# Optimization experiments

Hardware: AMD Instinct MI355X
Metric: run time of the kernel (lower is better)

Reference implementation:

```python
import jax, jax.numpy as jnp
import numpy as np

D = 64
H = 4
FF = 4  # fourier features
EPS = 1e-5


def _ln(x, g, b):
    m = jnp.mean(x, axis=-1, keepdims=True)
    v = jnp.mean((x - m) ** 2, axis=-1, keepdims=True)
    return (x - m) / jnp.sqrt(v + EPS) * g + b


def setup_inputs() -> dict:
    key = jax.random.key(0)
    ks = jax.random.split(key, 30)
    s = 0.05
    inp = {
        'feats': jax.random.normal(ks[0], (1, 1024, D), jnp.float32),
        'coors': jax.random.normal(ks[1], (1, 1024, 3), jnp.float32),
        'qkv_w': jax.random.normal(ks[2], (D, 3 * D), jnp.float32) * s,
        'out_w': jax.random.normal(ks[3], (D, D), jnp.float32) * s,
        'out_b': jnp.zeros((D,), jnp.float32),
        'edge_w1': jax.random.normal(ks[4], (2 * FF + 1, D), jnp.float32) * s,
        'edge_b1': jnp.zeros((D,), jnp.float32),
        'edge_w2': jax.random.normal(ks[5], (D, D), jnp.float32) * s,
        'edge_b2': jnp.zeros((D,), jnp.float32),
        'coord_w1': jax.random.normal(ks[6], (D, D), jnp.float32) * s,
        'coord_b1': jnp.zeros((D,), jnp.float32),
        'coord_w2': jax.random.normal(ks[7], (D, 1), jnp.float32) * s,
        'coord_b2': jnp.zeros((1,), jnp.float32),
        'gate_w1': jax.random.normal(ks[8], (D, D), jnp.float32) * s,
        'gate_b1': jnp.zeros((D,), jnp.float32),
        'gate_w2': jax.random.normal(ks[9], (D, 1), jnp.float32) * s,
        'gate_b2': jnp.zeros((1,), jnp.float32),
        'ln1_g': jnp.ones((D,), jnp.float32),
        'ln1_b': jnp.zeros((D,), jnp.float32),
        'ln2_g': jnp.ones((D,), jnp.float32),
        'ln2_b': jnp.zeros((D,), jnp.float32),
        'ffn_w1': jax.random.normal(ks[10], (D, 4 * D), jnp.float32) * s,
        'ffn_b1': jnp.zeros((4 * D,), jnp.float32),
        'ffn_w2': jax.random.normal(ks[11], (4 * D, D), jnp.float32) * s,
        'ffn_b2': jnp.zeros((D,), jnp.float32),
    }
    return inp


def reference(feats, coors, qkv_w, out_w, out_b, edge_w1, edge_b1, edge_w2, edge_b2,
              coord_w1, coord_b1, coord_w2, coord_b2, gate_w1, gate_b1, gate_w2, gate_b2,
              ln1_g, ln1_b, ln2_g, ln2_b, ffn_w1, ffn_b1, ffn_w2, ffn_b2):
    B, N, Dm = feats.shape
    x = _ln(feats, ln1_g, ln1_b)  # norm1 (pre-norm; also used as residual base, faithful to source)

    # pairwise relative coords and squared distance
    rel = coors[:, :, None, :] - coors[:, None, :, :]        # [B,N,N,3]
    rd = jnp.sum(rel ** 2, axis=-1, keepdims=True)            # [B,N,N,1]
    freqs = 2.0 ** jnp.arange(FF, dtype=coors.dtype)
    fr = rd / freqs                                           # [B,N,N,FF]
    enc = jnp.concatenate([jnp.sin(fr), jnp.cos(fr), rd], -1) # [B,N,N,2*FF+1]

    # edge MLP (edges=None, edge_dim=0)
    e_ij = jax.nn.silu(enc @ edge_w1 + edge_b1) @ edge_w2 + edge_b2  # [B,N,N,D]

    # attention
    qkv = x @ qkv_w
    q, k, v = jnp.split(qkv, 3, axis=-1)
    hd = Dm // H
    q = q.reshape(B, N, H, hd).transpose(0, 2, 1, 3)
    k = k.reshape(B, N, H, hd).transpose(0, 2, 1, 3)
    v = v.reshape(B, N, H, hd).transpose(0, 2, 1, 3)
    scores = jnp.einsum('bhid,bhjd->bhij', q, k) / jnp.sqrt(jnp.asarray(Dm, q.dtype))
    attn = jax.nn.softmax(scores, axis=-1)                    # [B,H,N,N]
    msg = jnp.einsum('bhij,bhjd->bhid', attn, v)
    msg = msg.transpose(0, 2, 1, 3).reshape(B, N, Dm)
    x = x + (msg @ out_w + out_b)
    x = x + (jax.nn.gelu(_ln(x, ln2_g, ln2_b) @ ffn_w1 + ffn_b1, approximate=False) @ ffn_w2 + ffn_b2)

    # coordinate update
    cw = (jax.nn.silu(e_ij @ coord_w1 + coord_b1) @ coord_w2 + coord_b2)[..., 0]  # [B,N,N]
    cw = cw * jnp.mean(attn, axis=1)
    gate = jax.nn.sigmoid(jax.nn.silu(x @ gate_w1 + gate_b1) @ gate_w2 + gate_b2)  # [B,N,1]
    delta = jnp.einsum('bij,bijd->bid', cw, rel) * gate
    return x, coors + delta
```

## Files before the change

kernel.cpp:

```cpp
#include <hip/hip_runtime.h>
#include <hip/hip_bf16.h>

#define N 1024
#define D 64

typedef __attribute__((ext_vector_type(8))) short bf16x8;
typedef __attribute__((ext_vector_type(4))) float f32x4;

__device__ __forceinline__ unsigned short f2b(float v) {
  unsigned u = __float_as_uint(v);
  u += 0x7fffu + ((u >> 16) & 1u);
  return (unsigned short)(u >> 16);
}
__device__ __forceinline__ unsigned short f2bc(float v) {
  union { __hip_bfloat16 h; unsigned short u; } r;
  r.h = __float2bfloat16(v);
  return r.u;
}
__device__ __forceinline__ unsigned pk2(float a, float b) {
  union { __hip_bfloat162 h; unsigned u; } r;
  r.h = __hip_bfloat162(__float2bfloat16(a), __float2bfloat16(b));
  return r.u;
}
__device__ __forceinline__ float bu(unsigned short u) {
  return __uint_as_float(((unsigned)u) << 16);
}
__device__ __forceinline__ float silu_f(float x) {
  return x * __builtin_amdgcn_rcpf(1.f + __expf(-x));
}
__device__ __forceinline__ float sigm_f(float x) {
  return __builtin_amdgcn_rcpf(1.f + __expf(-x));
}

__global__ __launch_bounds__(64) void k_ln1_qkv(
    const float* __restrict__ feats, const float* __restrict__ g, const float* __restrict__ b,
    const float* __restrict__ qkv_w, float* __restrict__ xn, float* __restrict__ qkv) {
  const int i = blockIdx.x, t = threadIdx.x;
  float v = feats[i * D + t];
  float s = v;
#pragma unroll
  for (int off = 32; off; off >>= 1) s += __shfl_xor(s, off);
  const float m = s * (1.0f / 64.0f);
  const float dv = v - m;
  float vs = dv * dv;
#pragma unroll
  for (int off = 32; off; off >>= 1) vs += __shfl_xor(vs, off);
  const float var = vs * (1.0f / 64.0f);
  const float xv = dv * rsqrtf(var + 1e-5f) * g[t] + b[t];
  xn[i * D + t] = xv;
  __shared__ float xs[D];
  xs[t] = xv;
  __syncthreads();
#pragma unroll
  for (int c = 0; c < 3; ++c) {
    const int col = t + c * 64;
    float acc = 0.f;
#pragma unroll 8
    for (int k = 0; k < D; ++k) acc += xs[k] * qkv_w[k * 192 + col];
    qkv[i * 192 + col] = acc;
  }
}

__global__ __launch_bounds__(256) void k_scores(
    const float* __restrict__ qkv, unsigned short* __restrict__ P,
    float* __restrict__ l_ws, float* __restrict__ pv_ws) {
  const int i0 = blockIdx.x * 64, j0 = blockIdx.y * 64, jb = blockIdx.y;
  const int t = threadIdx.x;
  const int lane = t & 63, h = t >> 6;
  const int l15 = lane & 15, lg = lane >> 4;
  const int r7 = l15 & 7;

  __shared__ __align__(16) unsigned short Qs[64 * 64];
  __shared__ __align__(16) unsigned short Ks[64 * 64];
  __shared__ __align__(16) unsigned short VTs[4 * 16 * 64];
  __shared__ __align__(16) unsigned short Ps[4 * 64 * 64];

  {
    const int si = t >> 2, q4 = t & 3;
    const int g0 = ((q4 * 2) ^ (si & 7)) * 8, g1 = ((q4 * 2 + 1) ^ (si & 7)) * 8;
    {
      const float* qr = &qkv[(i0 + si) * 192 + q4 * 16];
      float4 a0 = *(const float4*)(qr + 0), a1 = *(const float4*)(qr + 4);
      float4 a2 = *(const float4*)(qr + 8), a3 = *(const float4*)(qr + 12);
      *(uint4*)&Qs[si * 64 + g0] = make_uint4(
          pk2(a0.x * 0.125f, a0.y * 0.125f), pk2(a0.z * 0.125f, a0.w * 0.125f),
          pk2(a1.x * 0.125f, a1.y * 0.125f), pk2(a1.z * 0.125f, a1.w * 0.125f));
      *(uint4*)&Qs[si * 64 + g1] = make_uint4(
          pk2(a2.x * 0.125f, a2.y * 0.125f), pk2(a2.z * 0.125f, a2.w * 0.125f),
          pk2(a3.x * 0.125f, a3.y * 0.125f), pk2(a3.z * 0.125f, a3.w * 0.125f));
    }
    {
      const float* kr = &qkv[(j0 + si) * 192 + 64 + q4 * 16];
      float4 a0 = *(const float4*)(kr + 0), a1 = *(const float4*)(kr + 4);
      float4 a2 = *(const float4*)(kr + 8), a3 = *(const float4*)(kr + 12);
      *(uint4*)&Ks[si * 64 + g0] = make_uint4(pk2(a0.x, a0.y), pk2(a0.z, a0.w),
                                              pk2(a1.x, a1.y), pk2(a1.z, a1.w));
      *(uint4*)&Ks[si * 64 + g1] = make_uint4(pk2(a2.x, a2.y), pk2(a2.z, a2.w),
                                              pk2(a3.x, a3.y), pk2(a3.z, a3.w));
    }
    {
      const float* vr = &qkv[(j0 + si) * 192 + 128 + q4 * 16];
      float4 v0 = *(const float4*)(vr + 0), v1 = *(const float4*)(vr + 4);
      float4 v2 = *(const float4*)(vr + 8), v3 = *(const float4*)(vr + 12);
      float vv[16] = {v0.x, v0.y, v0.z, v0.w, v1.x, v1.y, v1.z, v1.w,
                      v2.x, v2.y, v2.z, v2.w, v3.x, v3.y, v3.z, v3.w};
      const int sj3 = si >> 3, sj7 = si & 7;
#pragma unroll
      for (int cc = 0; cc < 16; ++cc)
        VTs[q4 * 1024 + cc * 64 + ((sj3 ^ (cc & 7)) * 8) + sj7] = f2bc(vv[cc]);
    }
  }
  __syncthreads();

  const bf16x8 z8 = {0, 0, 0, 0, 0, 0, 0, 0};
  const int gk = ((h * 2 + (lg & 1)) ^ r7) * 8;
  bf16x8 qa[4], kb[4];
#pragma unroll
  for (int it = 0; it < 4; ++it) {
    qa[it] = *(const bf16x8*)&Qs[(it * 16 + l15) * 64 + gk];
    if (lg >= 2) qa[it] = z8;
    kb[it] = *(const bf16x8*)&Ks[(it * 16 + l15) * 64 + gk];
  }
  f32x4 acc[4][4];
#pragma unroll
  for (int it = 0; it < 4; ++it)
#pragma unroll
    for (int jt = 0; jt < 4; ++jt)
      acc[it][jt] = (f32x4){0.f, 0.f, 0.f, 0.f};
#pragma unroll
  for (int it = 0; it < 4; ++it)
#pragma unroll
    for (int jt = 0; jt < 4; ++jt)
      acc[it][jt] = __builtin_amdgcn_mfma_f32_16x16x32_bf16(qa[it], kb[jt], acc[it][jt], 0, 0, 0);

  float prow[4][4];
#pragma unroll
  for (int it = 0; it < 4; ++it)
#pragma unroll
    for (int rr = 0; rr < 4; ++rr) prow[it][rr] = 0.f;
#pragma unroll
  for (int it = 0; it < 4; ++it)
#pragma unroll
    for (int jt = 0; jt < 4; ++jt)
#pragma unroll
      for (int rr = 0; rr < 4; ++rr) {
        const float p = __expf(acc[it][jt][rr]);
        prow[it][rr] += p;
        const int irow = it * 16 + lg * 4 + rr;
        const int col = jt * 16 + l15;
        Ps[h * 4096 + irow * 64 + (((col >> 3) ^ (irow & 7)) * 8) + (col & 7)] = f2bc(p);
      }
#pragma unroll
  for (int it = 0; it < 4; ++it)
#pragma unroll
    for (int rr = 0; rr < 4; ++rr) {
      float s = prow[it][rr];
      s += __shfl_xor(s, 1); s += __shfl_xor(s, 2);
      s += __shfl_xor(s, 4); s += __shfl_xor(s, 8);
      if (l15 == 0)
        l_ws[h * 16384 + jb * 1024 + i0 + it * 16 + lg * 4 + rr] = s;
    }

  f32x4 av[4];
#pragma unroll
  for (int it = 0; it < 4; ++it) av[it] = (f32x4){0.f, 0.f, 0.f, 0.f};
#pragma unroll
  for (int ks = 0; ks < 2; ++ks) {
    const int gj = ((ks * 4 + lg) ^ r7) * 8;
    bf16x8 vb = *(const bf16x8*)&VTs[h * 1024 + l15 * 64 + gj];
#pragma unroll
    for (int it = 0; it < 4; ++it) {
      bf16x8 pa = *(const bf16x8*)&Ps[h * 4096 + (it * 16 + l15) * 64 + gj];
      av[it] = __builtin_amdgcn_mfma_f32_16x16x32_bf16(pa, vb, av[it], 0, 0, 0);
    }
  }
#pragma unroll
  for (int it = 0; it < 4; ++it)
#pragma unroll
    for (int rr = 0; rr < 4; ++rr)
      pv_ws[jb * 65536 + (i0 + it * 16 + lg * 4 + rr) * 64 + h * 16 + l15] = av[it][rr];

  {
    const int ir = t & 63;
    unsigned short* pg = &P[h * 1048576 + (i0 + ir) * 1024 + j0];
#pragma unroll
    for (int gg = 0; gg < 8; ++gg)
      *(uint4*)&pg[gg * 8] = *(const uint4*)&Ps[h * 4096 + ir * 64 + ((gg ^ (ir & 7)) * 8)];
  }
}

__global__ __launch_bounds__(256) void k_ffn_gate(
    const float* __restrict__ pv_ws, const float* __restrict__ l_ws,
    const float* __restrict__ xn,
    const float* __restrict__ out_w, const float* __restrict__ out_b,
    const float* __restrict__ ln2_g, const float* __restrict__ ln2_b,
    const float* __restrict__ fw1, const float* __restrict__ fb1,
    const float* __restrict__ fw2, const float* __restrict__ fb2,
    const float* __restrict__ gw1, const float* __restrict__ gb1,
    const float* __restrict__ gw2, const float* __restrict__ gb2,
    float* __restrict__ xout, float* __restrict__ gate) {
  const int i = blockIdx.x, t = threadIdx.x;
  __shared__ float msgv[64], xs[64], x1s[64], hs[256];
  if (t < 64) {
    float ls = 0.f;
#pragma unroll
    for (int jt = 0; jt < 16; ++jt) ls += l_ws[(t >> 4) * 16384 + jt * 1024 + i];
    const float invh = __builtin_amdgcn_rcpf(ls);
    float s = 0.f;
#pragma unroll
    for (int jt = 0; jt < 16; ++jt) s += pv_ws[jt * 65536 + i * 64 + t];
    msgv[t] = s * invh;
  }
  __syncthreads();
  if (t < 64) {
    float o = out_b[t];
#pragma unroll 8
    for (int k = 0; k < 64; ++k) o += msgv[k] * out_w[k * 64 + t];
    const float v = xn[i * 64 + t] + o;
    x1s[t] = v;
    float s = v;
#pragma unroll
    for (int off = 32; off; off >>= 1) s += __shfl_xor(s, off);
    const float m = s * (1.f / 64.f);
    const float dv = v - m;
    float vs = dv * dv;
#pragma unroll
    for (int off = 32; off; off >>= 1) vs += __shfl_xor(vs, off);
    xs[t] = dv * rsqrtf(vs * (1.f / 64.f) + 1e-5f) * ln2_g[t] + ln2_b[t];
  }
  __syncthreads();
  float a = fb1[t];
#pragma unroll 8
  for (int k = 0; k < 64; ++k) a += xs[k] * fw1[k * 256 + t];
  const float ge = 0.5f * a * (1.f + erff(a * 0.70710678118f));
  hs[t] = ge;
  __syncthreads();
  if (t < 64) {
    float o = fb2[t];
#pragma unroll 8
    for (int k = 0; k < 256; ++k) o += hs[k] * fw2[k * 64 + t];
    const float xo = x1s[t] + o;
    xout[i * 64 + t] = xo;
    xs[t] = xo;
  }
  __syncthreads();
  if (t < 64) {
    float a2 = gb1[t];
#pragma unroll 8
    for (int k = 0; k < 64; ++k) a2 += xs[k] * gw1[k * 64 + t];
    const float sg = a2 * sigm_f(a2);
    float pp = sg * gw2[t];
#pragma unroll
    for (int off = 32; off; off >>= 1) pp += __shfl_xor(pp, off);
    if (t == 0) gate[i] = sigm_f(pp + gb2[0]);
  }
}

__global__ __launch_bounds__(256) void k_prep(
    const float* __restrict__ ew1, const float* __restrict__ eb1,
    const float* __restrict__ ew2, const float* __restrict__ cw1,
    const float* __restrict__ eb2, const float* __restrict__ cb1,
    unsigned short* __restrict__ pw, float* __restrict__ b3p) {
  const int t = threadIdx.x;
  __shared__ float wc[64][64];
  for (int idx = t; idx < 4096; idx += 256) {
    const int r = idx >> 6, c = idx & 63;
    float s = 0.f;
#pragma unroll 8
    for (int k = 0; k < 64; ++k) s += ew2[r * 64 + k] * cw1[k * 64 + c];
    wc[r][c] = s;
  }
  __syncthreads();
  for (int idx = t; idx < 12 * 512; idx += 256) {
    const int e = idx & 7, l = (idx >> 3) & 63, f = idx >> 9;
    const int l15 = l & 15, lg = l >> 4;
    float v;
    if (f < 4) {
      const int d = f * 16 + l15, k = lg * 8 + e;
      v = (k < 9) ? ew1[k * 64 + d] : (k == 9 ? eb1[d] : 0.f);
    } else {
      const int g = f - 4, d = (g >> 1) * 16 + l15, k = (g & 1) * 32 + lg * 8 + e;
      v = wc[k][d];
    }
    pw[idx] = f2b(v);
  }
  if (t < 64) {
    float s = cb1[t];
#pragma unroll 8
    for (int k = 0; k < 64; ++k) s += eb2[k] * cw1[k * 64 + t];
    b3p[t] = s;
  }
}

__global__ __launch_bounds__(256, 2) void k_pair(
    const float* __restrict__ coors, const unsigned short* __restrict__ P,
    const float* __restrict__ l_ws, const unsigned short* __restrict__ pw,
    const float* __restrict__ b3p, const float* __restrict__ c2g,
    const float* __restrict__ cb2, float* __restrict__ partial) {
  const int i = blockIdx.x;
  const int half = blockIdx.y;
  const int t = threadIdx.x;
  const int w = t >> 6;
  const int lane = t & 63;
  const int l15 = lane & 15;
  const int lg = lane >> 4;

  __shared__ __align__(16) unsigned short buf[4][32][64];
  __shared__ float4 relma[4][32];
  __shared__ float invl_s[4];
  __shared__ float redb[4][3];

  if (t < 4) {
    float s = 0.f;
#pragma unroll
    for (int jt = 0; jt < 16; ++jt) s += l_ws[t * 16384 + jt * 1024 + i];
    invl_s[t] = 0.25f * __builtin_amdgcn_rcpf(s);
  }

  bf16x8 wf[12];
#pragma unroll
  for (int f = 0; f < 12; ++f)
    wf[f] = *(const bf16x8*)&pw[(f * 64 + lane) * 8];

  float b3v[16], c2v[16];
#pragma unroll
  for (int mt = 0; mt < 4; ++mt)
#pragma unroll
    for (int r = 0; r < 4; ++r) {
      const int d = mt * 16 + lg * 4 + r;
      b3v[mt * 4 + r] = b3p[d];
      c2v[mt * 4 + r] = c2g[d];
    }
  const float cb2q = cb2[0] * 0.25f;
  const float cix = coors[i * 3 + 0], ciy = coors[i * 3 + 1], ciz = coors[i * 3 + 2];

  if (lane < 32) {
    const int j = lane;
    unsigned short* rp = &buf[w][j][0];
    const uint4 z4 = make_uint4(0, 0, 0, 0);
    *(uint4*)&rp[(1 ^ (j & 7)) * 8] = z4;
    *(uint4*)&rp[(2 ^ (j & 7)) * 8] = z4;
    *(uint4*)&rp[(3 ^ (j & 7)) * 8] = z4;
  }
  __syncthreads();

  float dx = 0.f, dy = 0.f, dz = 0.f;
  f32x4 acc[4][2];

  for (int c = 0; c < 4; ++c) {
    {
      const int j = lane & 31;
      const int hhalf = lane >> 5;
      const int jg = half * 512 + c * 128 + w * 32 + j;
      const float rx = cix - coors[jg * 3 + 0];
      const float ry = ciy - coors[jg * 3 + 1];
      const float rz = ciz - coors[jg * 3 + 2];
      const float rd = rx * rx + ry * ry + rz * rz;
      unsigned short* rp = &buf[w][j][0];
      if (hhalf == 0) {
        const float p0 = bu(P[i * 1024 + jg]);
        const float p1 = bu(P[1048576 + i * 1024 + jg]);
        const float p2 = bu(P[2097152 + i * 1024 + jg]);
        const float p3 = bu(P[3145728 + i * 1024 + jg]);
        const float ma = p0 * invl_s[0] + p1 * invl_s[1] + p2 * invl_s[2] + p3 * invl_s[3];
        relma[w][j] = make_float4(ma * rx, ma * ry, ma * rz, 0.f);
        *(uint2*)&rp[(0 ^ (j & 7)) * 8] =
            make_uint2(pk2(__sinf(rd), __sinf(rd * 0.5f)),
                       pk2(__sinf(rd * 0.25f), __sinf(rd * 0.125f)));
        *(unsigned*)&rp[(1 ^ (j & 7)) * 8] = pk2(rd, 1.0f);
      } else {
        *(uint2*)&rp[((0 ^ (j & 7)) * 8) + 4] =
            make_uint2(pk2(__cosf(rd), __cosf(rd * 0.5f)),
                       pk2(__cosf(rd * 0.25f), __cosf(rd * 0.125f)));
      }
    }

#pragma unroll
    for (int mt = 0; mt < 4; ++mt)
#pragma unroll
      for (int nt = 0; nt < 2; ++nt)
        acc[mt][nt] = (f32x4){0.f, 0.f, 0.f, 0.f};
    {
      const int j0 = l15, j1 = 16 + l15;
      bf16x8 bf0 = *(const bf16x8*)&buf[w][j0][(lg ^ (j0 & 7)) * 8];
      bf16x8 bf1 = *(const bf16x8*)&buf[w][j1][(lg ^ (j1 & 7)) * 8];
#pragma unroll
      for (int mt = 0; mt < 4; ++mt) {
        acc[mt][0] = __builtin_amdgcn_mfma_f32_16x16x32_bf16(wf[mt], bf0, acc[mt][0], 0, 0, 0);
        acc[mt][1] = __builtin_amdgcn_mfma_f32_16x16x32_bf16(wf[mt], bf1, acc[mt][1], 0, 0, 0);
      }
    }
#pragma unroll
    for (int mt = 0; mt < 4; ++mt)
#pragma unroll
      for (int nt = 0; nt < 2; ++nt) {
        const f32x4 a = acc[mt][nt];
        const unsigned lo = pk2(silu_f(a[0]), silu_f(a[1]));
        const unsigned hi = pk2(silu_f(a[2]), silu_f(a[3]));
        const int j = nt * 16 + l15;
        const int g = mt * 2 + (lg >> 1);
        *(uint2*)&buf[w][j][((g ^ (j & 7)) * 8) + (lg & 1) * 4] = make_uint2(lo, hi);
      }

#pragma unroll
    for (int mt = 0; mt < 4; ++mt)
#pragma unroll
      for (int nt = 0; nt < 2; ++nt)
        acc[mt][nt] = (f32x4){b3v[mt * 4 + 0], b3v[mt * 4 + 1], b3v[mt * 4 + 2], b3v[mt * 4 + 3]};
#pragma unroll
    for (int ks = 0; ks < 2; ++ks) {
      const int gi = ks * 4 + lg;
      const int j0 = l15, j1 = 16 + l15;
      bf16x8 bf0 = *(const bf16x8*)&buf[w][j0][(gi ^ (j0 & 7)) * 8];
      bf16x8 bf1 = *(const bf16x8*)&buf[w][j1][(gi ^ (j1 & 7)) * 8];
#pragma unroll
      for (int mt = 0; mt < 4; ++mt) {
        acc[mt][0] = __builtin_amdgcn_mfma_f32_16x16x32_bf16(wf[4 + mt * 2 + ks], bf0, acc[mt][0], 0, 0, 0);
        acc[mt][1] = __builtin_amdgcn_mfma_f32_16x16x32_bf16(wf[4 + mt * 2 + ks], bf1, acc[mt][1], 0, 0, 0);
      }
    }

#pragma unroll
    for (int nt = 0; nt < 2; ++nt) {
      float cwp = cb2q;
#pragma unroll
      for (int mt = 0; mt < 4; ++mt) {
        const f32x4 a = acc[mt][nt];
#pragma unroll
        for (int r = 0; r < 4; ++r) cwp += silu_f(a[r]) * c2v[mt * 4 + r];
      }
      const float4 rm = relma[w][nt * 16 + l15];
      dx += cwp * rm.x;
      dy += cwp * rm.y;
      dz += cwp * rm.z;
    }
  }

#pragma unroll
  for (int off = 1; off < 64; off <<= 1) {
    dx += __shfl_xor(dx, off);
    dy += __shfl_xor(dy, off);
    dz += __shfl_xor(dz, off);
  }
  if (lane == 0) { redb[w][0] = dx; redb[w][1] = dy; redb[w][2] = dz; }
  __syncthreads();
  if (t == 0) {
    const int o = (i * 2 + half) * 3;
    partial[o + 0] = redb[0][0] + redb[1][0] + redb[2][0] + redb[3][0];
    partial[o + 1] = redb[0][1] + redb[1][1] + redb[2][1] + redb[3][1];
    partial[o + 2] = redb[0][2] + redb[1][2] + redb[2][2] + redb[3][2];
  }
}

__global__ __launch_bounds__(256) void k_finalize(
    const float* __restrict__ coors, const float* __restrict__ partial,
    const float* __restrict__ gate, float* __restrict__ outc) {
  const int i = blockIdx.x * 256 + threadIdx.x;
  if (i < N) {
    const float g = gate[i];
#pragma unroll
    for (int c = 0; c < 3; ++c)
      outc[i * 3 + c] = coors[i * 3 + c] + (partial[i * 6 + c] + partial[i * 6 + 3 + c]) * g;
  }
}

extern "C" void kernel_launch(void* const* d_in, const int* in_sizes, int n_in,
                              void* d_out, int out_size, void* d_ws, size_t ws_size,
                              hipStream_t stream) {
  const float* feats = (const float*)d_in[0];
  const float* coors = (const float*)d_in[1];
  const float* qkv_w = (const float*)d_in[2];
  const float* out_w = (const float*)d_in[3];
  const float* out_b = (const float*)d_in[4];
  const float* ew1 = (const float*)d_in[5];
  const float* eb1 = (const float*)d_in[6];
  const float* ew2 = (const float*)d_in[7];
  const float* eb2 = (const float*)d_in[8];
  const float* cw1 = (const float*)d_in[9];
  const float* cb1 = (const float*)d_in[10];
  const float* cw2 = (const float*)d_in[11];
  const float* cb2 = (const float*)d_in[12];
  const float* gw1 = (const float*)d_in[13];
  const float* gb1 = (const float*)d_in[14];
  const float* gw2 = (const float*)d_in[15];
  const float* gb2 = (const float*)d_in[16];
  const float* ln1_g = (const float*)d_in[17];
  const float* ln1_b = (const float*)d_in[18];
  const float* ln2_g = (const float*)d_in[19];
  const float* ln2_b = (const float*)d_in[20];
  const float* fw1 = (const float*)d_in[21];
  const float* fb1 = (const float*)d_in[22];
  const float* fw2 = (const float*)d_in[23];
  const float* fb2 = (const float*)d_in[24];

  float* ws = (float*)d_ws;
  float* xn = ws;
  float* qkv = ws + 65536;
  float* gate = ws + 262144;
  unsigned short* pw = (unsigned short*)(ws + 263168);
  float* b3p = ws + 267264;
  float* l_ws = ws + 267328;
  float* pv_ws = ws + 332864;
  float* partial = ws + 1381440;
  unsigned short* P = (unsigned short*)(ws + 1387584);

  float* xout = (float*)d_out;
  float* coorout = xout + 65536;

  hipLaunchKernelGGL(k_ln1_qkv, dim3(N), dim3(64), 0, stream, feats, ln1_g, ln1_b, qkv_w, xn, qkv);
  hipLaunchKernelGGL(k_prep, dim3(1), dim3(256), 0, stream, ew1, eb1, ew2, cw1, eb2, cb1, pw, b3p);
  hipLaunchKernelGGL(k_scores, dim3(16, 16), dim3(256), 0, stream, qkv, P, l_ws, pv_ws);
  hipLaunchKernelGGL(k_ffn_gate, dim3(N), dim3(256), 0, stream, pv_ws, l_ws, xn,
                     out_w, out_b, ln2_g, ln2_b,
                     fw1, fb1, fw2, fb2, gw1, gb1, gw2, gb2, xout, gate);
  hipLaunchKernelGGL(k_pair, dim3(N, 2), dim3(256), 0, stream, coors, P, l_ws, pw,
                     b3p, cw2, cb2, partial);
  hipLaunchKernelGGL(k_finalize, dim3(4), dim3(256), 0, stream, coors, partial, gate, coorout);
}
```

Measured before the change: 109.3 us.

## Exploit pairwise symmetry to halve edge MLP work in coordinate update

```diff
diff --git a/kernel.cpp b/kernel.cpp
--- a/kernel.cpp
+++ b/kernel.cpp
@@ -186,6 +186,67 @@
 #pragma unroll
     for (int gg = 0; gg < 8; ++gg)
       *(uint4*)&pg[gg * 8] = *(const uint4*)&Ps[h * 4096 + ir * 64 + ((gg ^ (ir & 7)) * 8)];
+  }
+}
+
+__global__ __launch_bounds__(256) void k_meanattn(
+    const unsigned short* P, const float* __restrict__ l_ws,
+    unsigned short* ma, unsigned short* __restrict__ maT) {
+  const int i0 = blockIdx.x * 64, j0 = blockIdx.y * 64;
+  const int t = threadIdx.x;
+  __shared__ float invl[4][64];
+  __shared__ unsigned short tile[64][68];
+  {
+    const int h = t >> 6, r = t & 63;
+    float s = 0.f;
+#pragma unroll
+    for (int jt = 0; jt < 16; ++jt) s += l_ws[h * 16384 + jt * 1024 + i0 + r];
+    invl[h][r] = 0.25f * __builtin_amdgcn_rcpf(s);
+  }
+  __syncthreads();
+  {
+    const int r = t >> 2, cg = t & 3;
+    float v[16];
+#pragma unroll
+    for (int k = 0; k < 16; ++k) v[k] = 0.f;
+#pragma unroll
+    for (int h = 0; h < 4; ++h) {
+      const unsigned short* pr = &P[h * 1048576 + (i0 + r) * 1024 + j0 + cg * 16];
+      uint4 a = *(const uint4*)pr;
+      uint4 b2 = *(const uint4*)(pr + 8);
+      const float sh = invl[h][r];
+      unsigned uu[8] = {a.x, a.y, a.z, a.w, b2.x, b2.y, b2.z, b2.w};
+#pragma unroll
+      for (int q = 0; q < 8; ++q) {
+        v[q * 2 + 0] += sh * bu((unsigned short)(uu[q] & 0xffffu));
+        v[q * 2 + 1] += sh * bu((unsigned short)(uu[q] >> 16));
+      }
+    }
+    unsigned out[8];
+#pragma unroll
+    for (int q = 0; q < 8; ++q) out[q] = pk2(v[2 * q], v[2 * q + 1]);
+    unsigned short* mr = &ma[(i0 + r) * 1024 + j0 + cg * 16];
+    *(uint4*)mr = make_uint4(out[0], out[1], out[2], out[3]);
+    *(uint4*)(mr + 8) = make_uint4(out[4], out[5], out[6], out[7]);
+#pragma unroll
+    for (int q = 0; q < 8; ++q) {
+      tile[r][cg * 16 + 2 * q] = (unsigned short)(out[q] & 0xffffu);
+      tile[r][cg * 16 + 2 * q + 1] = (unsigned short)(out[q] >> 16);
+    }
+  }
+  __syncthreads();
+  {
+    const int jr = t >> 2, icg = t & 3;
+    unsigned out[8];
+#pragma unroll
+    for (int q = 0; q < 8; ++q) {
+      const unsigned short lo = tile[icg * 16 + 2 * q][jr];
+      const unsigned short hi = tile[icg * 16 + 2 * q + 1][jr];
+      out[q] = (unsigned)lo | ((unsigned)hi << 16);
+    }
+    unsigned short* mtr = &maT[(j0 + jr) * 1024 + i0 + icg * 16];
+    *(uint4*)mtr = make_uint4(out[0], out[1], out[2], out[3]);
+    *(uint4*)(mtr + 8) = make_uint4(out[4], out[5], out[6], out[7]);
   }
 }
 
@@ -293,12 +354,17 @@
 }
 
 __global__ __launch_bounds__(256, 2) void k_pair(
-    const float* __restrict__ coors, const unsigned short* __restrict__ P,
-    const float* __restrict__ l_ws, const unsigned short* __restrict__ pw,
+    const float* __restrict__ coors,
+    const unsigned short* __restrict__ ma, const unsigned short* __restrict__ maT,
+    const unsigned short* __restrict__ pw,
     const float* __restrict__ b3p, const float* __restrict__ c2g,
     const float* __restrict__ cb2, float* __restrict__ partial) {
-  const int i = blockIdx.x;
-  const int half = blockIdx.y;
+  int bb = blockIdx.x, ti = 0;
+  while (bb >= 32 - ti) { bb -= 32 - ti; ++ti; }
+  const int tj = ti + bb;
+  const bool diag = (ti == tj);
+  const int nch = diag ? 4 : 8;
+
   const int t = threadIdx.x;
   const int w = t >> 6;
   const int lane = t & 63;
@@ -306,16 +372,8 @@
   const int lg = lane >> 4;
 
   __shared__ __align__(16) unsigned short buf[4][32][64];
-  __shared__ float4 relma[4][32];
-  __shared__ float invl_s[4];
-  __shared__ float redb[4][3];
-
-  if (t < 4) {
-    float s = 0.f;
-#pragma unroll
-    for (int jt = 0; jt < 16; ++jt) s += l_ws[t * 16384 + jt * 1024 + i];
-    invl_s[t] = 0.25f * __builtin_amdgcn_rcpf(s);
-  }
+  __shared__ float4 relA[4][32], relB[4][32];
+  __shared__ float di[4][32][3], dj[4][32][3];
 
   bf16x8 wf[12];
 #pragma unroll
@@ -332,44 +390,45 @@
       c2v[mt * 4 + r] = c2g[d];
     }
   const float cb2q = cb2[0] * 0.25f;
-  const float cix = coors[i * 3 + 0], ciy = coors[i * 3 + 1], ciz = coors[i * 3 + 2];
 
   if (lane < 32) {
     const int j = lane;
+#pragma unroll
+    for (int k2 = 0; k2 < 3; ++k2) { di[w][j][k2] = 0.f; dj[w][j][k2] = 0.f; }
     unsigned short* rp = &buf[w][j][0];
     const uint4 z4 = make_uint4(0, 0, 0, 0);
     *(uint4*)&rp[(1 ^ (j & 7)) * 8] = z4;
     *(uint4*)&rp[(2 ^ (j & 7)) * 8] = z4;
     *(uint4*)&rp[(3 ^ (j & 7)) * 8] = z4;
   }
-  __syncthreads();
-
-  float dx = 0.f, dy = 0.f, dz = 0.f;
+
   f32x4 acc[4][2];
 
-  for (int c = 0; c < 4; ++c) {
+  for (int c = 0; c < nch; ++c) {
+    const int dgn = diag ? (c * 4 + w + 1) : (c * 4 + w);
     {
-      const int j = lane & 31;
+      const int p = lane & 31;
       const int hhalf = lane >> 5;
-      const int jg = half * 512 + c * 128 + w * 32 + j;
-      const float rx = cix - coors[jg * 3 + 0];
-      const float ry = ciy - coors[jg * 3 + 1];
-      const float rz = ciz - coors[jg * 3 + 2];
+      const int ig = ti * 32 + p;
+      const int jj = (p + dgn) & 31;
+      const int jg = tj * 32 + jj;
+      const float rx = coors[ig * 3 + 0] - coors[jg * 3 + 0];
+      const float ry = coors[ig * 3 + 1] - coors[jg * 3 + 1];
+      const float rz = coors[ig * 3 + 2] - coors[jg * 3 + 2];
       const float rd = rx * rx + ry * ry + rz * rz;
-      unsigned short* rp = &buf[w][j][0];
+      unsigned short* rp = &buf[w][p][0];
       if (hhalf == 0) {
-        const float p0 = bu(P[i * 1024 + jg]);
-        const float p1 = bu(P[1048576 + i * 1024 + jg]);
-        const float p2 = bu(P[2097152 + i * 1024 + jg]);
-        const float p3 = bu(P[3145728 + i * 1024 + jg]);
-        const float ma = p0 * invl_s[0] + p1 * invl_s[1] + p2 * invl_s[2] + p3 * invl_s[3];
-        relma[w][j] = make_float4(ma * rx, ma * ry, ma * rz, 0.f);
-        *(uint2*)&rp[(0 ^ (j & 7)) * 8] =
+        float mi = bu(ma[ig * 1024 + jg]);
+        float mj = bu(maT[ig * 1024 + jg]);
+        if (diag && dgn == 16 && p >= 16) { mi = 0.f; mj = 0.f; }
+        relA[w][p] = make_float4(mi * rx, mi * ry, mi * rz, 0.f);
+        relB[w][p] = make_float4(mj * rx, mj * ry, mj * rz, 0.f);
+        *(uint2*)&rp[(0 ^ (p & 7)) * 8] =
             make_uint2(pk2(__sinf(rd), __sinf(rd * 0.5f)),
                        pk2(__sinf(rd * 0.25f), __sinf(rd * 0.125f)));
-        *(unsigned*)&rp[(1 ^ (j & 7)) * 8] = pk2(rd, 1.0f);
+        *(unsigned*)&rp[(1 ^ (p & 7)) * 8] = pk2(rd, 1.0f);
       } else {
-        *(uint2*)&rp[((0 ^ (j & 7)) * 8) + 4] =
+        *(uint2*)&rp[((0 ^ (p & 7)) * 8) + 4] =
             make_uint2(pk2(__cosf(rd), __cosf(rd * 0.5f)),
                        pk2(__cosf(rd * 0.25f), __cosf(rd * 0.125f)));
       }
@@ -429,38 +488,49 @@
 #pragma unroll
         for (int r = 0; r < 4; ++r) cwp += silu_f(a[r]) * c2v[mt * 4 + r];
       }
-      const float4 rm = relma[w][nt * 16 + l15];
-      dx += cwp * rm.x;
-      dy += cwp * rm.y;
-      dz += cwp * rm.z;
-    }
-  }
-
-#pragma unroll
-  for (int off = 1; off < 64; off <<= 1) {
-    dx += __shfl_xor(dx, off);
-    dy += __shfl_xor(dy, off);
-    dz += __shfl_xor(dz, off);
-  }
-  if (lane == 0) { redb[w][0] = dx; redb[w][1] = dy; redb[w][2] = dz; }
-  __syncthreads();
-  if (t == 0) {
-    const int o = (i * 2 + half) * 3;
-    partial[o + 0] = redb[0][0] + redb[1][0] + redb[2][0] + redb[3][0];
-    partial[o + 1] = redb[0][1] + redb[1][1] + redb[2][1] + redb[3][1];
-    partial[o + 2] = redb[0][2] + redb[1][2] + redb[2][2] + redb[3][2];
+      cwp += __shfl_xor(cwp, 16);
+      cwp += __shfl_xor(cwp, 32);
+      if (lg == 0) {
+        const int p = nt * 16 + l15;
+        const int jj = (p + dgn) & 31;
+        const float4 rA = relA[w][p];
+        const float4 rB = relB[w][p];
+        di[w][p][0] += cwp * rA.x; di[w][p][1] += cwp * rA.y; di[w][p][2] += cwp * rA.z;
+        dj[w][jj][0] -= cwp * rB.x; dj[w][jj][1] -= cwp * rB.y; dj[w][jj][2] -= cwp * rB.z;
+      }
+    }
+  }
+
+  __syncthreads();
+  if (!diag) {
+    if (t < 96) {
+      const int p = t / 3, k = t % 3;
+      const float s = di[0][p][k] + di[1][p][k] + di[2][p][k] + di[3][p][k];
+      partial[tj * 3072 + (ti * 32 + p) * 3 + k] = s;
+    } else if (t < 192) {
+      const int u = t - 96, q = u / 3, k = u % 3;
+      const float s = dj[0][q][k] + dj[1][q][k] + dj[2][q][k] + dj[3][q][k];
+      partial[ti * 3072 + (tj * 32 + q) * 3 + k] = s;
+    }
+  } else {
+    if (t < 96) {
+      const int p = t / 3, k = t % 3;
+      const float s = di[0][p][k] + di[1][p][k] + di[2][p][k] + di[3][p][k]
+                    + dj[0][p][k] + dj[1][p][k] + dj[2][p][k] + dj[3][p][k];
+      partial[ti * 3072 + (ti * 32 + p) * 3 + k] = s;
+    }
   }
 }
 
 __global__ __launch_bounds__(256) void k_finalize(
     const float* __restrict__ coors, const float* __restrict__ partial,
     const float* __restrict__ gate, float* __restrict__ outc) {
-  const int i = blockIdx.x * 256 + threadIdx.x;
-  if (i < N) {
-    const float g = gate[i];
-#pragma unroll
-    for (int c = 0; c < 3; ++c)
-      outc[i * 3 + c] = coors[i * 3 + c] + (partial[i * 6 + c] + partial[i * 6 + 3 + c]) * g;
+  const int idx = blockIdx.x * 256 + threadIdx.x;
+  if (idx < 3072) {
+    float s = 0.f;
+#pragma unroll
+    for (int sl = 0; sl < 32; ++sl) s += partial[sl * 3072 + idx];
+    outc[idx] = coors[idx] + s * gate[idx / 3];
   }
 }
 
@@ -498,11 +568,13 @@
   float* qkv = ws + 65536;
   float* gate = ws + 262144;
   unsigned short* pw = (unsigned short*)(ws + 263168);
-  float* b3p = ws + 267264;
-  float* l_ws = ws + 267328;
-  float* pv_ws = ws + 332864;
-  float* partial = ws + 1381440;
-  unsigned short* P = (unsigned short*)(ws + 1387584);
+  float* b3p = ws + 266240;
+  float* l_ws = ws + 266304;
+  float* pv_ws = ws + 331840;
+  float* partial = ws + 1380416;
+  unsigned short* P = (unsigned short*)(ws + 1478720);
+  unsigned short* ma = P;
+  unsigned short* maT = (unsigned short*)(ws + 3575872);
 
   float* xout = (float*)d_out;
   float* coorout = xout + 65536;
@@ -510,10 +582,11 @@
   hipLaunchKernelGGL(k_ln1_qkv, dim3(N), dim3(64), 0, stream, feats, ln1_g, ln1_b, qkv_w, xn, qkv);
   hipLaunchKernelGGL(k_prep, dim3(1), dim3(256), 0, stream, ew1, eb1, ew2, cw1, eb2, cb1, pw, b3p);
   hipLaunchKernelGGL(k_scores, dim3(16, 16), dim3(256), 0, stream, qkv, P, l_ws, pv_ws);
+  hipLaunchKernelGGL(k_meanattn, dim3(16, 16), dim3(256), 0, stream, P, l_ws, ma, maT);
   hipLaunchKernelGGL(k_ffn_gate, dim3(N), dim3(256), 0, stream, pv_ws, l_ws, xn,
                      out_w, out_b, ln2_g, ln2_b,
                      fw1, fb1, fw2, fb2, gw1, gb1, gw2, gb2, xout, gate);
-  hipLaunchKernelGGL(k_pair, dim3(N, 2), dim3(256), 0, stream, coors, P, l_ws, pw,
+  hipLaunchKernelGGL(k_pair, dim3(528), dim3(256), 0, stream, coors, ma, maT, pw,
                      b3p, cw2, cb2, partial);
-  hipLaunchKernelGGL(k_finalize, dim3(4), dim3(256), 0, stream, coors, partial, gate, coorout);
-}
+  hipLaunchKernelGGL(k_finalize, dim3(12), dim3(256), 0, stream, coors, partial, gate, coorout);
+}
```

Result: faster. 105.2 us (-3.8%).
